# Performance work log

Measured on AMD Instinct MI355X. Metric: run time of the kernel, lower is better.

The kernel has to match this reference:

```python
import jax, jax.numpy as jnp
import numpy as np

B, T, D, H, K = 2, 384, 512, 8, 48
HD = D // H  # head_dim = 64
LN_EPS = 1e-5


def setup_inputs() -> dict:
    key = jax.random.key(0)
    ks = jax.random.split(key, 6)
    def lin_w(k, out_d, in_d):
        return jax.random.normal(k, (out_d, in_d), jnp.float32) / np.sqrt(in_d).astype(np.float32)
    return {
        "x": jax.random.normal(ks[0], (B, T, D), jnp.float32),
        "g_w": lin_w(ks[1], H, D), "g_b": jnp.zeros((H,), jnp.float32),
        "sp_w": lin_w(ks[2], D, HD), "sp_b": jnp.zeros((D,), jnp.float32),
        "gate_w": lin_w(ks[3], D, D), "gate_b": jnp.zeros((D,), jnp.float32),
        "U_w": lin_w(ks[4], D, D), "U_b": jnp.zeros((D,), jnp.float32),
        "ln_g": jnp.ones((D,), jnp.float32), "ln_b": jnp.zeros((D,), jnp.float32),
    }


def reference(x, g_w, g_b, sp_w, sp_b, gate_w, gate_b, U_w, U_b, ln_g, ln_b):
    b, t, d = x.shape
    # head-split superposition
    phi = x.reshape(b, t, H, HD)                               # (B,T,H,hd)
    alpha = jax.nn.softmax(x @ g_w.T + g_b, axis=-1)           # (B,T,H)
    x_super = jnp.einsum('bth,bthd->btd', alpha, phi)          # (B,T,hd)
    x_super = x_super @ sp_w.T + sp_b                          # (B,T,D)
    # gated pairwise entanglement: interaction[b,i,j,:] = gate[b,i]*gate[b,j]
    gate = jax.nn.sigmoid(x_super @ gate_w.T + gate_b)         # (B,T,D)
    interaction = gate[:, :, None, :] * gate[:, None, :, :]    # (B,T,T,D)
    # top-k by L2 norm over feature dim, gather along j axis
    scores = jnp.sqrt(jnp.sum(interaction * interaction, axis=-1))  # (B,T,T)
    _, idx = jax.lax.top_k(scores, K)                          # (B,T,K)
    gathered = jnp.take_along_axis(interaction, idx[..., None], axis=2)  # (B,T,K,D)
    entangled = gathered.sum(axis=2)                           # (B,T,D)
    x_out = x_super + entangled
    y = x_out @ U_w.T + U_b
    mu = jnp.mean(y, axis=-1, keepdims=True)
    var = jnp.mean((y - mu) ** 2, axis=-1, keepdims=True)
    return ln_g * (y - mu) * jax.lax.rsqrt(var + LN_EPS) + ln_b
```

## Files before the change

### kernel.cpp

```cpp
#include <hip/hip_runtime.h>
#include <math.h>
#include <float.h>

#define T_ 384
#define D_ 512
#define H_ 8
#define HD_ 64
#define K_ 48
#define LN_EPS 1e-5f
#define NTOK 768
#define PSTRIDE (NTOK * D_)
#define T2 (T_ * T_)

__global__ __launch_bounds__(256) void k_super_m(
    const float* __restrict__ x, const float* __restrict__ g_w,
    const float* __restrict__ g_b, const float* __restrict__ sp_w,
    const float* __restrict__ sp_b, const float* __restrict__ gate_w,
    const float* __restrict__ gate_b, float* __restrict__ xs,
    float* __restrict__ hd_g, float* __restrict__ MT, float* __restrict__ Mb) {
    __shared__ float xsh[D_];
    __shared__ float logits[H_];
    __shared__ float hdv[HD_];
    int bid = blockIdx.x, tid = threadIdx.x;
    if (bid < NTOK) {
        const float* xt = x + (size_t)bid * D_;
        ((float2*)xsh)[tid] = ((const float2*)xt)[tid];
        __syncthreads();
        int h = tid >> 5, l = tid & 31;
        float p = 0.f;
#pragma unroll
        for (int i = 0; i < 16; ++i) {
            int k = l + 32 * i;
            p += xsh[k] * g_w[h * D_ + k];
        }
#pragma unroll
        for (int off = 16; off > 0; off >>= 1) p += __shfl_xor(p, off);
        if (l == 0) logits[h] = p + g_b[h];
        __syncthreads();
        if (tid < HD_) {
            float m = logits[0];
#pragma unroll
            for (int hh = 1; hh < H_; ++hh) m = fmaxf(m, logits[hh]);
            float e[H_];
            float sum = 0.f;
#pragma unroll
            for (int hh = 0; hh < H_; ++hh) { e[hh] = expf(logits[hh] - m); sum += e[hh]; }
            float inv = 1.f / sum;
            float v = 0.f;
#pragma unroll
            for (int hh = 0; hh < H_; ++hh) v += e[hh] * inv * xsh[hh * HD_ + tid];
            hdv[tid] = v;
            hd_g[(size_t)bid * HD_ + tid] = v;
        }
        __syncthreads();
        float a0 = sp_b[tid], a1 = sp_b[tid + 256];
        const float* w0 = sp_w + (size_t)tid * HD_;
        const float* w1 = sp_w + (size_t)(tid + 256) * HD_;
#pragma unroll
        for (int k = 0; k < HD_; k += 4) {
            float4 h4 = *(const float4*)&hdv[k];
            float4 u0 = *(const float4*)&w0[k];
            float4 u1 = *(const float4*)&w1[k];
            a0 += h4.x * u0.x + h4.y * u0.y + h4.z * u0.z + h4.w * u0.w;
            a1 += h4.x * u1.x + h4.y * u1.y + h4.z * u1.z + h4.w * u1.w;
        }
        xs[(size_t)bid * D_ + tid] = a0;
        xs[(size_t)bid * D_ + 256 + tid] = a1;
    } else {
        int d = (bid - NTOK) * 4 + (tid >> 6);
        int l = tid & 63;
        const float* gw = gate_w + (size_t)d * D_;
        float p = 0.f;
#pragma unroll
        for (int i = 0; i < 8; ++i) p += gw[l + 64 * i] * sp_b[l + 64 * i];
#pragma unroll
        for (int off = 32; off > 0; off >>= 1) p += __shfl_xor(p, off);
        if (l == 0) Mb[d] = p + gate_b[d];
        float acc = 0.f;
        for (int k = 0; k < D_; k += 4) {
            float4 a4 = *(const float4*)&gw[k];
            acc += a4.x * sp_w[(k + 0) * HD_ + l] + a4.y * sp_w[(k + 1) * HD_ + l] +
                   a4.z * sp_w[(k + 2) * HD_ + l] + a4.w * sp_w[(k + 3) * HD_ + l];
        }
        MT[(size_t)l * D_ + d] = acc;
    }
}

__global__ __launch_bounds__(256) void k_gate(const float* __restrict__ hd_g,
                                              const float* __restrict__ MT,
                                              const float* __restrict__ Mb,
                                              float* __restrict__ gate) {
    int bid = blockIdx.x, tid = threadIdx.x;
    int t0 = (bid >> 3) * 8, c0 = (bid & 7) * 64;
    int rr = tid >> 6, c = tid & 63;
    int ta = t0 + rr, tb = t0 + rr + 4;
    const float4* hd4 = (const float4*)hd_g;
    float acc0 = 0.f, acc1 = 0.f;
#pragma unroll
    for (int j4 = 0; j4 < 16; ++j4) {
        float4 h0 = hd4[ta * 16 + j4];
        float4 h1 = hd4[tb * 16 + j4];
        int j = j4 * 4;
        float m0 = MT[(size_t)(j + 0) * D_ + c0 + c];
        float m1 = MT[(size_t)(j + 1) * D_ + c0 + c];
        float m2 = MT[(size_t)(j + 2) * D_ + c0 + c];
        float m3 = MT[(size_t)(j + 3) * D_ + c0 + c];
        acc0 += h0.x * m0 + h0.y * m1 + h0.z * m2 + h0.w * m3;
        acc1 += h1.x * m0 + h1.y * m1 + h1.z * m2 + h1.w * m3;
    }
    float mb = Mb[c0 + c];
    gate[(size_t)ta * D_ + c0 + c] = 1.f / (1.f + expf(-(acc0 + mb)));
    gate[(size_t)tb * D_ + c0 + c] = 1.f / (1.f + expf(-(acc1 + mb)));
}

__global__ __launch_bounds__(256) void k_scores_part(const float* __restrict__ gate,
                                                     float* __restrict__ spart) {
    int z = blockIdx.z;
    int b = z >> 3, ks = z & 7;
    int kbase = ks * 64;
    int i0 = blockIdx.y * 64, j0 = blockIdx.x * 64;
    int tid = threadIdx.x;
    int tx = tid & 15, ty = tid >> 4;
    __shared__ float Ash[16][68];
    __shared__ float Bsh[16][68];
    float acc[4][4];
#pragma unroll
    for (int r = 0; r < 4; ++r)
#pragma unroll
        for (int c = 0; c < 4; ++c) acc[r][c] = 0.f;
    const float* gb = gate + (size_t)b * T_ * D_;
    int sr = tid >> 2, sc4 = (tid & 3) * 4;
    for (int k0 = kbase; k0 < kbase + 64; k0 += 16) {
        float4 av = *(const float4*)&gb[(size_t)(i0 + sr) * D_ + k0 + sc4];
        float4 bvv = *(const float4*)&gb[(size_t)(j0 + sr) * D_ + k0 + sc4];
        Ash[sc4 + 0][sr] = av.x * av.x;
        Ash[sc4 + 1][sr] = av.y * av.y;
        Ash[sc4 + 2][sr] = av.z * av.z;
        Ash[sc4 + 3][sr] = av.w * av.w;
        Bsh[sc4 + 0][sr] = bvv.x * bvv.x;
        Bsh[sc4 + 1][sr] = bvv.y * bvv.y;
        Bsh[sc4 + 2][sr] = bvv.z * bvv.z;
        Bsh[sc4 + 3][sr] = bvv.w * bvv.w;
        __syncthreads();
#pragma unroll
        for (int kk = 0; kk < 16; ++kk) {
            float4 a4 = *(const float4*)&Ash[kk][4 * ty];
            float4 b4 = *(const float4*)&Bsh[kk][4 * tx];
            float ar[4] = {a4.x, a4.y, a4.z, a4.w};
            float bc[4] = {b4.x, b4.y, b4.z, b4.w};
#pragma unroll
            for (int r = 0; r < 4; ++r)
#pragma unroll
                for (int c = 0; c < 4; ++c) acc[r][c] += ar[r] * bc[c];
        }
        __syncthreads();
    }
    float* sp = spart + (size_t)z * T2;
#pragma unroll
    for (int r = 0; r < 4; ++r) {
        float4 o;
        o.x = acc[r][0];
        o.y = acc[r][1];
        o.z = acc[r][2];
        o.w = acc[r][3];
        *(float4*)&sp[(size_t)(i0 + 4 * ty + r) * T_ + j0 + 4 * tx] = o;
    }
}

__global__ __launch_bounds__(256) void k_topk_ent(const float* __restrict__ spart,
                                                  const float* __restrict__ gate,
                                                  const float* __restrict__ xs,
                                                  float* __restrict__ xo) {
    __shared__ float s[T_];
    __shared__ int sel[K_];
    int row = blockIdx.x, tid = threadIdx.x;
    int b = row / T_;
    int i = row - b * T_;
    for (int j = tid; j < T_; j += 256) {
        float acc = 0.f;
#pragma unroll
        for (int ks = 0; ks < 8; ++ks)
            acc += spart[(size_t)(b * 8 + ks) * T2 + (size_t)i * T_ + j];
        s[j] = acc;
    }
    __syncthreads();
    for (int j = tid; j < T_; j += 256) {
        float v = s[j];
        int cnt = 0;
        for (int j2 = 0; j2 < T_; ++j2) {
            float u = s[j2];
            cnt += (u > v) || (u == v && j2 < j);
        }
        if (cnt < K_) sel[cnt] = j;
    }
    __syncthreads();
    const float2* g2 = (const float2*)gate;
    float2 sum = {0.f, 0.f};
    int rb = b * T_;
    for (int n = 0; n < K_; ++n) {
        int j = sel[n];
        float2 g = g2[(size_t)(rb + j) * 256 + tid];
        sum.x += g.x;
        sum.y += g.y;
    }
    float2 gi = g2[(size_t)row * 256 + tid];
    float2 xv = ((const float2*)xs)[(size_t)row * 256 + tid];
    float2 o;
    o.x = xv.x + gi.x * sum.x;
    o.y = xv.y + gi.y * sum.y;
    ((float2*)xo)[(size_t)row * 256 + tid] = o;
}

__global__ __launch_bounds__(256) void k_wgemm_part(const float* __restrict__ in,
                                                    const float* __restrict__ W,
                                                    float* __restrict__ part) {
    int c0 = blockIdx.x * 64, r0 = blockIdx.y * 32;
    int kbase = blockIdx.z * 128;
    float* pout = part + (size_t)blockIdx.z * PSTRIDE;
    int tid = threadIdx.x;
    int ry = tid >> 4, cx = tid & 15;
    __shared__ float A_shT[32][33];
    __shared__ float B_sh[32][65];
    float acc[2][4];
#pragma unroll
    for (int r = 0; r < 2; ++r)
#pragma unroll
        for (int c = 0; c < 4; ++c) acc[r][c] = 0.f;
    int asr = tid >> 3, asc = (tid & 7) * 4;
    int bsr = tid >> 2, bsk = (tid & 3) * 8;
    for (int k0 = kbase; k0 < kbase + 128; k0 += 32) {
        float4 a4 = *(const float4*)&in[(size_t)(r0 + asr) * D_ + k0 + asc];
        A_shT[asc + 0][asr] = a4.x;
        A_shT[asc + 1][asr] = a4.y;
        A_shT[asc + 2][asr] = a4.z;
        A_shT[asc + 3][asr] = a4.w;
        float4 b4a = *(const float4*)&W[(size_t)(c0 + bsr) * D_ + k0 + bsk];
        float4 b4b = *(const float4*)&W[(size_t)(c0 + bsr) * D_ + k0 + bsk + 4];
        B_sh[bsk + 0][bsr] = b4a.x;
        B_sh[bsk + 1][bsr] = b4a.y;
        B_sh[bsk + 2][bsr] = b4a.z;
        B_sh[bsk + 3][bsr] = b4a.w;
        B_sh[bsk + 4][bsr] = b4b.x;
        B_sh[bsk + 5][bsr] = b4b.y;
        B_sh[bsk + 6][bsr] = b4b.z;
        B_sh[bsk + 7][bsr] = b4b.w;
        __syncthreads();
#pragma unroll
        for (int kk = 0; kk < 32; ++kk) {
            float2 a2 = *(const float2*)&A_shT[kk][ry * 2];
            float4 b4 = *(const float4*)&B_sh[kk][cx * 4];
            acc[0][0] += a2.x * b4.x; acc[0][1] += a2.x * b4.y;
            acc[0][2] += a2.x * b4.z; acc[0][3] += a2.x * b4.w;
            acc[1][0] += a2.y * b4.x; acc[1][1] += a2.y * b4.y;
            acc[1][2] += a2.y * b4.z; acc[1][3] += a2.y * b4.w;
        }
        __syncthreads();
    }
#pragma unroll
    for (int r = 0; r < 2; ++r) {
        float4 o;
        o.x = acc[r][0];
        o.y = acc[r][1];
        o.z = acc[r][2];
        o.w = acc[r][3];
        *(float4*)&pout[(size_t)(r0 + ry * 2 + r) * D_ + c0 + cx * 4] = o;
    }
}

__global__ __launch_bounds__(256) void k_wred_ln(const float* __restrict__ part,
                                                 const float* __restrict__ U_b,
                                                 const float* __restrict__ ln_g,
                                                 const float* __restrict__ ln_b,
                                                 float* __restrict__ out) {
    int tid = threadIdx.x;
    int idx = blockIdx.x * 256 + tid;
    const float4* p = (const float4*)part;
    float4 s = {0.f, 0.f, 0.f, 0.f};
#pragma unroll
    for (int q = 0; q < 4; ++q) {
        float4 a = p[idx + q * (PSTRIDE / 4)];
        s.x += a.x; s.y += a.y; s.z += a.z; s.w += a.w;
    }
    float4 ub = ((const float4*)U_b)[tid & 127];
    s.x += ub.x; s.y += ub.y; s.z += ub.z; s.w += ub.w;
    float sum = s.x + s.y + s.z + s.w;
    float sq = s.x * s.x + s.y * s.y + s.z * s.z + s.w * s.w;
#pragma unroll
    for (int off = 32; off > 0; off >>= 1) {
        sum += __shfl_xor(sum, off);
        sq += __shfl_xor(sq, off);
    }
    __shared__ float red[4][2];
    int wave = tid >> 6;
    if ((tid & 63) == 0) { red[wave][0] = sum; red[wave][1] = sq; }
    __syncthreads();
    int rw = (tid >> 7) * 2;
    float m1 = red[rw][0] + red[rw + 1][0];
    float m2 = red[rw][1] + red[rw + 1][1];
    float mu = m1 * (1.f / D_);
    float var = fmaxf(m2 * (1.f / D_) - mu * mu, 0.f);
    float inv = rsqrtf(var + LN_EPS);
    float4 lg = ((const float4*)ln_g)[tid & 127];
    float4 lb = ((const float4*)ln_b)[tid & 127];
    float4 o;
    o.x = lg.x * (s.x - mu) * inv + lb.x;
    o.y = lg.y * (s.y - mu) * inv + lb.y;
    o.z = lg.z * (s.z - mu) * inv + lb.z;
    o.w = lg.w * (s.w - mu) * inv + lb.w;
    ((float4*)out)[idx] = o;
}

extern "C" void kernel_launch(void* const* d_in, const int* in_sizes, int n_in,
                              void* d_out, int out_size, void* d_ws, size_t ws_size,
                              hipStream_t stream) {
    const float* x      = (const float*)d_in[0];
    const float* g_w    = (const float*)d_in[1];
    const float* g_b    = (const float*)d_in[2];
    const float* sp_w   = (const float*)d_in[3];
    const float* sp_b   = (const float*)d_in[4];
    const float* gate_w = (const float*)d_in[5];
    const float* gate_b = (const float*)d_in[6];
    const float* U_w    = (const float*)d_in[7];
    const float* U_b    = (const float*)d_in[8];
    const float* ln_g   = (const float*)d_in[9];
    const float* ln_b   = (const float*)d_in[10];

    float* ws    = (float*)d_ws;
    float* xs    = ws;
    float* gate  = xs + PSTRIDE;
    float* xo    = gate + PSTRIDE;
    float* hd_g  = xo + PSTRIDE;
    float* MT    = hd_g + 49152;
    float* Mb    = MT + 32768;
    float* part  = Mb + 512;
    float* spart = part + 4 * PSTRIDE;

    k_super_m<<<NTOK + 128, 256, 0, stream>>>(x, g_w, g_b, sp_w, sp_b, gate_w,
                                              gate_b, xs, hd_g, MT, Mb);
    k_gate<<<NTOK, 256, 0, stream>>>(hd_g, MT, Mb, gate);
    k_scores_part<<<dim3(T_ / 64, T_ / 64, 16), 256, 0, stream>>>(gate, spart);
    k_topk_ent<<<NTOK, 256, 0, stream>>>(spart, gate, xs, xo);
    k_wgemm_part<<<dim3(D_ / 64, NTOK / 32, 4), 256, 0, stream>>>(xo, U_w, part);
    k_wred_ln<<<NTOK * D_ / 1024, 256, 0, stream>>>(part, U_b, ln_g, ln_b, (float*)d_out);
}
```

Before: 166.6 us.

## Fuse split-K reduction and LayerNorm into GEMM via last-block atomic counter

Merges the final split-K GEMM and the separate reduce+LayerNorm kernel into one launch. Each block atomically bumps a per-row-tile counter, and the last of the 32 blocks for a 32-row tile sums the 4 partials, adds the bias and applies LayerNorm. This removes one kernel launch and its dependency gap. In exchange, one block per row tile does the reduction serially over 32 rows, and the counter is never reset; it relies on modulo-32 wraparound, which stays correct across repeated calls.

```diff
diff --git a/kernel.cpp b/kernel.cpp
--- a/kernel.cpp
+++ b/kernel.cpp
@@ -11,6 +11,8 @@
 #define NTOK 768
 #define PSTRIDE (NTOK * D_)
 #define T2 (T_ * T_)
+
+__device__ unsigned g_ctr[24];
 
 __global__ __launch_bounds__(256) void k_super_m(
     const float* __restrict__ x, const float* __restrict__ g_w,
@@ -211,9 +213,11 @@
     ((float2*)xo)[(size_t)row * 256 + tid] = o;
 }
 
-__global__ __launch_bounds__(256) void k_wgemm_part(const float* __restrict__ in,
-                                                    const float* __restrict__ W,
-                                                    float* __restrict__ part) {
+__global__ __launch_bounds__(256) void k_wgemm_ln(
+    const float* __restrict__ in, const float* __restrict__ W,
+    const float* __restrict__ U_b, const float* __restrict__ ln_g,
+    const float* __restrict__ ln_b, float* __restrict__ part,
+    float* __restrict__ out) {
     int c0 = blockIdx.x * 64, r0 = blockIdx.y * 32;
     int kbase = blockIdx.z * 128;
     float* pout = part + (size_t)blockIdx.z * PSTRIDE;
@@ -265,49 +269,62 @@
         o.w = acc[r][3];
         *(float4*)&pout[(size_t)(r0 + ry * 2 + r) * D_ + c0 + cx * 4] = o;
     }
-}
-
-__global__ __launch_bounds__(256) void k_wred_ln(const float* __restrict__ part,
-                                                 const float* __restrict__ U_b,
-                                                 const float* __restrict__ ln_g,
-                                                 const float* __restrict__ ln_b,
-                                                 float* __restrict__ out) {
-    int tid = threadIdx.x;
-    int idx = blockIdx.x * 256 + tid;
-    const float4* p = (const float4*)part;
-    float4 s = {0.f, 0.f, 0.f, 0.f};
-#pragma unroll
-    for (int q = 0; q < 4; ++q) {
-        float4 a = p[idx + q * (PSTRIDE / 4)];
-        s.x += a.x; s.y += a.y; s.z += a.z; s.w += a.w;
-    }
-    float4 ub = ((const float4*)U_b)[tid & 127];
-    s.x += ub.x; s.y += ub.y; s.z += ub.z; s.w += ub.w;
-    float sum = s.x + s.y + s.z + s.w;
-    float sq = s.x * s.x + s.y * s.y + s.z * s.z + s.w * s.w;
-#pragma unroll
-    for (int off = 32; off > 0; off >>= 1) {
-        sum += __shfl_xor(sum, off);
-        sq += __shfl_xor(sq, off);
-    }
-    __shared__ float red[4][2];
-    int wave = tid >> 6;
-    if ((tid & 63) == 0) { red[wave][0] = sum; red[wave][1] = sq; }
+    __threadfence();
     __syncthreads();
-    int rw = (tid >> 7) * 2;
-    float m1 = red[rw][0] + red[rw + 1][0];
-    float m2 = red[rw][1] + red[rw + 1][1];
-    float mu = m1 * (1.f / D_);
-    float var = fmaxf(m2 * (1.f / D_) - mu * mu, 0.f);
-    float inv = rsqrtf(var + LN_EPS);
-    float4 lg = ((const float4*)ln_g)[tid & 127];
-    float4 lb = ((const float4*)ln_b)[tid & 127];
-    float4 o;
-    o.x = lg.x * (s.x - mu) * inv + lb.x;
-    o.y = lg.y * (s.y - mu) * inv + lb.y;
-    o.z = lg.z * (s.z - mu) * inv + lb.z;
-    o.w = lg.w * (s.w - mu) * inv + lb.w;
-    ((float4*)out)[idx] = o;
+    __shared__ int isLast;
+    if (tid == 0) {
+        unsigned t = __hip_atomic_fetch_add(&g_ctr[blockIdx.y], 1u,
+                                            __ATOMIC_ACQ_REL, __HIP_MEMORY_SCOPE_AGENT);
+        isLast = ((t & 31u) == 31u);
+    }
+    __syncthreads();
+    if (!isLast) return;
+    __threadfence();
+    int lane = tid & 63, wv = tid >> 6;
+    const float4* p4 = (const float4*)part;
+    const float4* ub4 = (const float4*)U_b;
+    const float4* lg4 = (const float4*)ln_g;
+    const float4* lb4 = (const float4*)ln_b;
+    float4* out4 = (float4*)out;
+    for (int g = 0; g < 8; ++g) {
+        int r = r0 + g * 4 + wv;
+        size_t base = (size_t)r * (D_ / 4) + lane * 2;
+        float4 s0 = {0.f, 0.f, 0.f, 0.f}, s1 = {0.f, 0.f, 0.f, 0.f};
+#pragma unroll
+        for (int q = 0; q < 4; ++q) {
+            float4 a = p4[base + (size_t)q * (PSTRIDE / 4)];
+            float4 bq = p4[base + 1 + (size_t)q * (PSTRIDE / 4)];
+            s0.x += a.x;  s0.y += a.y;  s0.z += a.z;  s0.w += a.w;
+            s1.x += bq.x; s1.y += bq.y; s1.z += bq.z; s1.w += bq.w;
+        }
+        float4 u0 = ub4[lane * 2], u1 = ub4[lane * 2 + 1];
+        s0.x += u0.x; s0.y += u0.y; s0.z += u0.z; s0.w += u0.w;
+        s1.x += u1.x; s1.y += u1.y; s1.z += u1.z; s1.w += u1.w;
+        float sum = s0.x + s0.y + s0.z + s0.w + s1.x + s1.y + s1.z + s1.w;
+        float sq = s0.x * s0.x + s0.y * s0.y + s0.z * s0.z + s0.w * s0.w +
+                   s1.x * s1.x + s1.y * s1.y + s1.z * s1.z + s1.w * s1.w;
+#pragma unroll
+        for (int off = 32; off > 0; off >>= 1) {
+            sum += __shfl_xor(sum, off);
+            sq += __shfl_xor(sq, off);
+        }
+        float mu = sum * (1.f / D_);
+        float var = fmaxf(sq * (1.f / D_) - mu * mu, 0.f);
+        float inv = rsqrtf(var + LN_EPS);
+        float4 g0 = lg4[lane * 2], g1 = lg4[lane * 2 + 1];
+        float4 b0 = lb4[lane * 2], b1 = lb4[lane * 2 + 1];
+        float4 o0, o1;
+        o0.x = g0.x * (s0.x - mu) * inv + b0.x;
+        o0.y = g0.y * (s0.y - mu) * inv + b0.y;
+        o0.z = g0.z * (s0.z - mu) * inv + b0.z;
+        o0.w = g0.w * (s0.w - mu) * inv + b0.w;
+        o1.x = g1.x * (s1.x - mu) * inv + b1.x;
+        o1.y = g1.y * (s1.y - mu) * inv + b1.y;
+        o1.z = g1.z * (s1.z - mu) * inv + b1.z;
+        o1.w = g1.w * (s1.w - mu) * inv + b1.w;
+        out4[base] = o0;
+        out4[base + 1] = o1;
+    }
 }
 
 extern "C" void kernel_launch(void* const* d_in, const int* in_sizes, int n_in,
@@ -340,6 +357,6 @@
     k_gate<<<NTOK, 256, 0, stream>>>(hd_g, MT, Mb, gate);
     k_scores_part<<<dim3(T_ / 64, T_ / 64, 16), 256, 0, stream>>>(gate, spart);
     k_topk_ent<<<NTOK, 256, 0, stream>>>(spart, gate, xs, xo);
-    k_wgemm_part<<<dim3(D_ / 64, NTOK / 32, 4), 256, 0, stream>>>(xo, U_w, part);
-    k_wred_ln<<<NTOK * D_ / 1024, 256, 0, stream>>>(part, U_b, ln_g, ln_b, (float*)d_out);
-}
+    k_wgemm_ln<<<dim3(D_ / 64, NTOK / 32, 4), 256, 0, stream>>>(
+        xo, U_w, U_b, ln_g, ln_b, part, (float*)d_out);
+}
```

New measurement: 257.9 us. +54.8%, slower.
